# Performance work log

Measured on AMD Instinct MI355X. Metric: run time of the kernel, lower is better.

## Reference

```python
import jax, jax.numpy as jnp
import numpy as np
import math

B, S, HID = 2, 1024, 2048
NH, HD = 16, 128
STREAM_R, SELECT_R, RECENT_R = 0.02, 0.06, 0.08
FF = 0.9  # forgetting factor
ROPE_BASE = 10000.0


def setup_inputs() -> dict:
    key = jax.random.key(0)
    ks = jax.random.split(key, 5)
    return {
        "hidden_states": jax.random.normal(ks[0], (B, S, HID), dtype=jnp.float32),
        "wq": jax.random.normal(ks[1], (HID, HID), dtype=jnp.float32) * 0.02,
        "wk": jax.random.normal(ks[2], (HID, HID), dtype=jnp.float32) * 0.02,
        "wv": jax.random.normal(ks[3], (HID, HID), dtype=jnp.float32) * 0.02,
        "wo": jax.random.normal(ks[4], (HID, HID), dtype=jnp.float32) * 0.02,
    }


def _rope_tables(seq_len, dim):
    inv_freq = 1.0 / (ROPE_BASE ** (jnp.arange(0, dim, 2, dtype=jnp.float32) / dim))
    freqs = jnp.outer(jnp.arange(seq_len, dtype=jnp.float32), inv_freq)  # [S, D/2]
    emb = jnp.concatenate([freqs, freqs], axis=-1)  # [S, D]
    return jnp.cos(emb), jnp.sin(emb)


def _rotate_half(x):
    x1, x2 = jnp.split(x, 2, axis=-1)
    return jnp.concatenate([-x2, x1], axis=-1)


def a2s_base_mask(attn_weights, sb, selb, rb, ff):
    # attn_weights: [B,H,S,S] (causal mask already added). Returns bool keep-mask [B,H,S,S].
    Bv, Hv, Sq, Sk = attn_weights.shape
    scores = jax.nn.softmax(attn_weights.astype(jnp.float32), axis=-1)  # [B,H,S,S]
    cb = sb + selb + rb  # cache budget
    # EMA warmup over first cb rows: sum_i ff^(cb-1-i) * scores[i]
    w = ff ** jnp.arange(cb - 1, -1, -1, dtype=jnp.float32)
    select0 = jnp.einsum('t,bhts->bhs', w, scores[:, :, :cb, :])
    mask0 = jnp.ones((Bv, Hv, Sk), dtype=bool)
    pos = jnp.arange(Sk)

    xs_scores = jnp.moveaxis(scores[:, :, cb:Sk - 1, :], 2, 0)  # [T,B,H,S]
    ts = jnp.arange(cb, Sk - 1, dtype=jnp.int32)

    def step(carry, inp):
        sel, m = carry
        sc, t = inp
        cur = sc * m
        cur = cur / jnp.sum(cur, axis=-1, keepdims=True)
        sel = ff * sel + cur
        local = t - rb
        # argmin over window [sb : local+1]; outside -> +inf (evicted entries already +inf)
        win = jnp.where((pos >= sb) & (pos <= local), sel, jnp.inf)
        mi = jnp.argmin(win, axis=-1)  # [B,H], first-min like torch
        evict = pos == mi[..., None]  # [B,H,S] one-hot bool
        sel = jnp.where(evict, jnp.inf, sel)
        m_new = m & ~evict
        return (sel, m_new), m_new

    _, rows = jax.lax.scan(step, (select0, mask0), (xs_scores, ts))
    head = jnp.ones((Bv, Hv, cb + 1, Sk), dtype=bool)  # rows 0..cb stay all-True
    tail = jnp.moveaxis(rows, 0, 2)  # rows cb+1..S-1
    return jnp.concatenate([head, tail], axis=2)


def reference(hidden_states, wq, wk, wv, wo):
    sb = math.floor(STREAM_R * S + 0.5)
    selb = math.floor(SELECT_R * S + 0.5)
    rb = math.floor(RECENT_R * S + 0.5)

    q = (hidden_states @ wq).reshape(B, S, NH, HD).transpose(0, 2, 1, 3)
    k = (hidden_states @ wk).reshape(B, S, NH, HD).transpose(0, 2, 1, 3)
    v = (hidden_states @ wv).reshape(B, S, NH, HD).transpose(0, 2, 1, 3)

    cos, sin = _rope_tables(S, HD)  # [S,HD]
    q = q * cos + _rotate_half(q) * sin
    k = k * cos + _rotate_half(k) * sin

    attn = jnp.einsum('bhqd,bhkd->bhqk', q, k) / math.sqrt(HD)
    mask_val = jnp.finfo(jnp.float32).min
    causal = jnp.where(jnp.tril(jnp.ones((S, S), dtype=bool)), 0.0, mask_val)[None, None]
    attn = jnp.maximum(attn + causal, mask_val)

    keep = a2s_base_mask(jax.lax.stop_gradient(attn), sb, selb, rb, FF)
    attn = jnp.where(keep, attn, mask_val)  # torch.min(attention_mask) == mask_val

    probs = jax.nn.softmax(attn.astype(jnp.float32), axis=-1).astype(q.dtype)
    out = jnp.einsum('bhqk,bhkd->bhqd', probs, v)
    out = out.transpose(0, 2, 1, 3).reshape(B, S, HID)
    return out @ wo
```

## Files before the change

kernel.cpp:

```cpp
#include <hip/hip_runtime.h>
#include <math.h>

#define Bb    2
#define Ss    1024
#define HIDd  2048
#define NHh   16
#define HDd   128
#define SBc   20
#define SELBc 61
#define RBc   82
#define CBc   163
#define FFf   0.9f
#define MASKVAL (-3.4028234663852886e38f)
#define NBH   (Bb*NHh)
#define NROWS (NBH*Ss)

typedef __attribute__((ext_vector_type(8))) short short8;
typedef __attribute__((ext_vector_type(4))) float f32x4;

__device__ __forceinline__ unsigned short f2b(float f) {
    unsigned u = __float_as_uint(f);
    u = (u + 0x7FFFu + ((u >> 16) & 1u)) >> 16;
    return (unsigned short)u;
}
__device__ __forceinline__ float b2f(unsigned short h) {
    return __uint_as_float((unsigned)h << 16);
}

#if defined(__has_builtin)
#if __has_builtin(__builtin_amdgcn_global_load_lds)
#define USE_GLD 1
#endif
#endif

__device__ __forceinline__ void gload16(const void* g, void* l) {
#ifdef USE_GLD
    __builtin_amdgcn_global_load_lds(
        (const __attribute__((address_space(1))) void*)g,
        (__attribute__((address_space(3))) void*)l, 16, 0, 0);
#else
    *(short8*)l = *(const short8*)g;
#endif
}

__global__ __launch_bounds__(256) void conv_split(const float* __restrict__ x,
                                                  unsigned short* __restrict__ yh,
                                                  unsigned short* __restrict__ yl, int n4)
{
    int i = blockIdx.x * 256 + threadIdx.x;
    if (i >= n4) return;
    float4 v = ((const float4*)x)[i];
    ushort4 h, l;
    h.x = f2b(v.x); l.x = f2b(v.x - b2f(h.x));
    h.y = f2b(v.y); l.y = f2b(v.y - b2f(h.y));
    h.z = f2b(v.z); l.z = f2b(v.z - b2f(h.z));
    h.w = f2b(v.w); l.w = f2b(v.w - b2f(h.w));
    ((ushort4*)yh)[i] = h;
    ((ushort4*)yl)[i] = l;
}

__global__ __launch_bounds__(256) void tconv_all(const float* __restrict__ wq,
                                                 const float* __restrict__ wk,
                                                 const float* __restrict__ wv,
                                                 const float* __restrict__ wo,
                                                 unsigned short* __restrict__ wqth,
                                                 unsigned short* __restrict__ wqtl,
                                                 unsigned short* __restrict__ wkth,
                                                 unsigned short* __restrict__ wktl,
                                                 unsigned short* __restrict__ wvt,
                                                 unsigned short* __restrict__ wot)
{
    __shared__ float T[64][65];
    const int z = blockIdx.z;
    const float* W = (z == 0) ? wq : (z == 1) ? wk : (z == 2) ? wv : wo;
    int n0 = blockIdx.x * 64, k0 = blockIdx.y * 64;
    int tid = threadIdx.x;
    int rr = tid >> 4, cc = (tid & 15) * 4;
#pragma unroll
    for (int p = 0; p < 4; ++p) {
        int r = rr + p * 16;
        float4 x = *(const float4*)&W[(size_t)(k0 + r) * HIDd + n0 + cc];
        T[r][cc] = x.x; T[r][cc + 1] = x.y; T[r][cc + 2] = x.z; T[r][cc + 3] = x.w;
    }
    __syncthreads();
    if (z < 2) {
        unsigned short* Wth = z ? wkth : wqth;
        unsigned short* Wtl = z ? wktl : wqtl;
#pragma unroll
        for (int p = 0; p < 4; ++p) {
            int rn = rr + p * 16;
            float v0 = T[cc][rn], v1 = T[cc + 1][rn], v2 = T[cc + 2][rn], v3 = T[cc + 3][rn];
            ushort4 h, l;
            h.x = f2b(v0); l.x = f2b(v0 - b2f(h.x));
            h.y = f2b(v1); l.y = f2b(v1 - b2f(h.y));
            h.z = f2b(v2); l.z = f2b(v2 - b2f(h.z));
            h.w = f2b(v3); l.w = f2b(v3 - b2f(h.w));
            *(ushort4*)&Wth[(size_t)(n0 + rn) * HIDd + k0 + cc] = h;
            *(ushort4*)&Wtl[(size_t)(n0 + rn) * HIDd + k0 + cc] = l;
        }
    } else {
        unsigned short* Wt = (z == 2) ? wvt : wot;
#pragma unroll
        for (int p = 0; p < 4; ++p) {
            int rn = rr + p * 16;
            ushort4 o;
            o.x = f2b(T[cc][rn]);     o.y = f2b(T[cc + 1][rn]);
            o.z = f2b(T[cc + 2][rn]); o.w = f2b(T[cc + 3][rn]);
            *(ushort4*)&Wt[(size_t)(n0 + rn) * HIDd + k0 + cc] = o;
        }
    }
}

__global__ __launch_bounds__(256) void gemm_qkv(const unsigned short* __restrict__ hsh,
                                                const unsigned short* __restrict__ hsl,
                                                const unsigned short* __restrict__ wqth,
                                                const unsigned short* __restrict__ wqtl,
                                                const unsigned short* __restrict__ wkth,
                                                const unsigned short* __restrict__ wktl,
                                                const unsigned short* __restrict__ wvt,
                                                float* __restrict__ qf,
                                                float* __restrict__ kf,
                                                float* __restrict__ vf)
{
    __shared__ unsigned short AsH[128 * 32], AsL[128 * 32];
    __shared__ unsigned short BsH[128 * 32], BsL[128 * 32];
    const int tid = threadIdx.x;
    const int region = blockIdx.x >> 4;
    const int bn = (blockIdx.x & 15) * 128;
    const int bm = blockIdx.y * 128;
    const int K = HIDd;
    const int lane = tid & 63, wid = tid >> 6;
    const int wr = (wid >> 1) * 64, wc = (wid & 1) * 64;
    const int lm = lane & 15, lk = (lane >> 4) * 8;
    const int lr = (lane >> 4) * 4;

    f32x4 acc[4][4];
#pragma unroll
    for (int mi = 0; mi < 4; ++mi)
#pragma unroll
        for (int ni = 0; ni < 4; ++ni) acc[mi][ni] = 0.0f;

    if (region < 2) {
        const unsigned short* Bh = region ? wkth : wqth;
        const unsigned short* Bl = region ? wktl : wqtl;
        float* C = region ? kf : qf;
        for (int k0 = 0; k0 < K; k0 += 32) {
#pragma unroll
            for (int l = 0; l < 2; ++l) {
                int L = tid + l * 256;
                int row = L >> 2, c8 = (L & 3) * 8;
                size_t ga = (size_t)(bm + row) * K + k0 + c8;
                size_t gb = (size_t)(bn + row) * K + k0 + c8;
                gload16(&hsh[ga], &AsH[L * 8]);
                gload16(&hsl[ga], &AsL[L * 8]);
                gload16(&Bh[gb], &BsH[L * 8]);
                gload16(&Bl[gb], &BsL[L * 8]);
            }
            __syncthreads();
            short8 ah[4], al[4], bh[4], bl[4];
#pragma unroll
            for (int mi = 0; mi < 4; ++mi) {
                ah[mi] = *(short8*)&AsH[(wr + mi * 16 + lm) * 32 + lk];
                al[mi] = *(short8*)&AsL[(wr + mi * 16 + lm) * 32 + lk];
            }
#pragma unroll
            for (int ni = 0; ni < 4; ++ni) {
                bh[ni] = *(short8*)&BsH[(wc + ni * 16 + lm) * 32 + lk];
                bl[ni] = *(short8*)&BsL[(wc + ni * 16 + lm) * 32 + lk];
            }
#pragma unroll
            for (int mi = 0; mi < 4; ++mi)
#pragma unroll
                for (int ni = 0; ni < 4; ++ni) {
                    acc[mi][ni] = __builtin_amdgcn_mfma_f32_16x16x32_bf16(ah[mi], bh[ni], acc[mi][ni], 0, 0, 0);
                    acc[mi][ni] = __builtin_amdgcn_mfma_f32_16x16x32_bf16(ah[mi], bl[ni], acc[mi][ni], 0, 0, 0);
                    acc[mi][ni] = __builtin_amdgcn_mfma_f32_16x16x32_bf16(al[mi], bh[ni], acc[mi][ni], 0, 0, 0);
                }
            __syncthreads();
        }
#pragma unroll
        for (int mi = 0; mi < 4; ++mi)
#pragma unroll
            for (int ni = 0; ni < 4; ++ni)
#pragma unroll
                for (int r = 0; r < 4; ++r) {
                    int m = bm + wr + mi * 16 + lr + r;
                    int n = bn + wc + ni * 16 + lm;
                    int b_ = m / Ss, s_ = m % Ss;
                    int h_ = n / HDd, d_ = n % HDd;
                    C[(size_t)((b_ * NHh + h_) * Ss + s_) * HDd + d_] = acc[mi][ni][r];
                }
    } else {
        for (int k0 = 0; k0 < K; k0 += 32) {
#pragma unroll
            for (int l = 0; l < 2; ++l) {
                int L = tid + l * 256;
                int row = L >> 2, c8 = (L & 3) * 8;
                gload16(&hsh[(size_t)(bm + row) * K + k0 + c8], &AsH[L * 8]);
                gload16(&wvt[(size_t)(bn + row) * K + k0 + c8], &BsH[L * 8]);
            }
            __syncthreads();
            short8 af[4], bf[4];
#pragma unroll
            for (int mi = 0; mi < 4; ++mi) af[mi] = *(short8*)&AsH[(wr + mi * 16 + lm) * 32 + lk];
#pragma unroll
            for (int ni = 0; ni < 4; ++ni) bf[ni] = *(short8*)&BsH[(wc + ni * 16 + lm) * 32 + lk];
#pragma unroll
            for (int mi = 0; mi < 4; ++mi)
#pragma unroll
                for (int ni = 0; ni < 4; ++ni)
                    acc[mi][ni] = __builtin_amdgcn_mfma_f32_16x16x32_bf16(af[mi], bf[ni], acc[mi][ni], 0, 0, 0);
            __syncthreads();
        }
#pragma unroll
        for (int mi = 0; mi < 4; ++mi)
#pragma unroll
            for (int ni = 0; ni < 4; ++ni)
#pragma unroll
                for (int r = 0; r < 4; ++r) {
                    int m = bm + wr + mi * 16 + lr + r;
                    int n = bn + wc + ni * 16 + lm;
                    int b_ = m / Ss, s_ = m % Ss;
                    int h_ = n / HDd, d_ = n % HDd;
                    vf[(size_t)((b_ * NHh + h_) * Ss + s_) * HDd + d_] = acc[mi][ni][r];
                }
    }
}

__global__ __launch_bounds__(256) void gemm_bf16t(const unsigned short* __restrict__ A,
                                                  const unsigned short* __restrict__ Bt,
                                                  float* __restrict__ C,
                                                  int M, int N, int K)
{
    __shared__ unsigned short As[128 * 32];
    __shared__ unsigned short Bs[128 * 32];
    const int tid = threadIdx.x;
    const int bm = blockIdx.y * 128, bn = blockIdx.x * 128;
    const int lane = tid & 63, wid = tid >> 6;
    const int wr = (wid >> 1) * 64, wc = (wid & 1) * 64;
    const int lm = lane & 15, lk = (lane >> 4) * 8;

    f32x4 acc[4][4];
#pragma unroll
    for (int mi = 0; mi < 4; ++mi)
#pragma unroll
        for (int ni = 0; ni < 4; ++ni) acc[mi][ni] = 0.0f;

    for (int k0 = 0; k0 < K; k0 += 32) {
#pragma unroll
        for (int l = 0; l < 2; ++l) {
            int L = tid + l * 256;
            int row = L >> 2, c8 = (L & 3) * 8;
            gload16(&A[(size_t)(bm + row) * K + k0 + c8], &As[L * 8]);
            gload16(&Bt[(size_t)(bn + row) * K + k0 + c8], &Bs[L * 8]);
        }
        __syncthreads();
        short8 af[4], bf[4];
#pragma unroll
        for (int mi = 0; mi < 4; ++mi) af[mi] = *(short8*)&As[(wr + mi * 16 + lm) * 32 + lk];
#pragma unroll
        for (int ni = 0; ni < 4; ++ni) bf[ni] = *(short8*)&Bs[(wc + ni * 16 + lm) * 32 + lk];
#pragma unroll
        for (int mi = 0; mi < 4; ++mi)
#pragma unroll
            for (int ni = 0; ni < 4; ++ni)
                acc[mi][ni] = __builtin_amdgcn_mfma_f32_16x16x32_bf16(af[mi], bf[ni], acc[mi][ni], 0, 0, 0);
        __syncthreads();
    }
    const int lr = (lane >> 4) * 4;
#pragma unroll
    for (int mi = 0; mi < 4; ++mi)
#pragma unroll
        for (int ni = 0; ni < 4; ++ni)
#pragma unroll
            for (int r = 0; r < 4; ++r) {
                int m = bm + wr + mi * 16 + lr + r;
                int n = bn + wc + ni * 16 + lm;
                C[(size_t)m * N + n] = acc[mi][ni][r];
            }
}

__global__ __launch_bounds__(64) void rope_qk_split(const float* __restrict__ q,
                                                    const float* __restrict__ k,
                                                    unsigned short* __restrict__ qh,
                                                    unsigned short* __restrict__ ql,
                                                    unsigned short* __restrict__ kh,
                                                    unsigned short* __restrict__ kl)
{
    int idx = blockIdx.x;
    int s = idx % Ss;
    int d = threadIdx.x;
    float inv = powf(10000.0f, -2.0f * (float)d / 128.0f);
    float fr = (float)s * inv;
    float c = cosf(fr), sn = sinf(fr);
    size_t base = (size_t)idx * HDd;
    float q1 = q[base + d], q2 = q[base + d + 64];
    float k1 = k[base + d], k2 = k[base + d + 64];
    float qa = q1 * c - q2 * sn, qbv = q2 * c + q1 * sn;
    float ka = k1 * c - k2 * sn, kbv = k2 * c + k1 * sn;
    unsigned short h;
    h = f2b(qa);  qh[base + d]      = h; ql[base + d]      = f2b(qa  - b2f(h));
    h = f2b(qbv); qh[base + d + 64] = h; ql[base + d + 64] = f2b(qbv - b2f(h));
    h = f2b(ka);  kh[base + d]      = h; kl[base + d]      = f2b(ka  - b2f(h));
    h = f2b(kbv); kh[base + d + 64] = h; kl[base + d + 64] = f2b(kbv - b2f(h));
}

__global__ __launch_bounds__(256) void attn_qk_split(const unsigned short* __restrict__ qh,
                                                     const unsigned short* __restrict__ ql,
                                                     const unsigned short* __restrict__ kh,
                                                     const unsigned short* __restrict__ kl,
                                                     float* __restrict__ attn)
{
    const int bh = blockIdx.z;
    const int bm = blockIdx.y * 128, bn = blockIdx.x * 128;
    float* C = attn + (size_t)bh * Ss * Ss;
    const int tid = threadIdx.x;

    if (blockIdx.x > blockIdx.y) return;

    const size_t hb = (size_t)bh * Ss * HDd;
    const unsigned short* Ah = qh + hb;
    const unsigned short* Al = ql + hb;
    const unsigned short* Bh = kh + hb;
    const unsigned short* Bl = kl + hb;

    __shared__ unsigned short AsH[128 * 32], AsL[128 * 32];
    __shared__ unsigned short BsH[128 * 32], BsL[128 * 32];
    const int lane = tid & 63, wid = tid >> 6;
    const int wr = (wid >> 1) * 64, wc = (wid & 1) * 64;
    const int lm = lane & 15, lk = (lane >> 4) * 8;

    f32x4 acc[4][4];
#pragma unroll
    for (int mi = 0; mi < 4; ++mi)
#pragma unroll
        for (int ni = 0; ni < 4; ++ni) acc[mi][ni] = 0.0f;

    for (int k0 = 0; k0 < HDd; k0 += 32) {
#pragma unroll
        for (int l = 0; l < 2; ++l) {
            int L = tid + l * 256;
            int row = L >> 2, c8 = (L & 3) * 8;
            size_t ga = (size_t)(bm + row) * HDd + k0 + c8;
            size_t gb = (size_t)(bn + row) * HDd + k0 + c8;
            gload16(&Ah[ga], &AsH[L * 8]);
            gload16(&Al[ga], &AsL[L * 8]);
            gload16(&Bh[gb], &BsH[L * 8]);
            gload16(&Bl[gb], &BsL[L * 8]);
        }
        __syncthreads();
        short8 ah[4], al[4], bh2[4], bl2[4];
#pragma unroll
        for (int mi = 0; mi < 4; ++mi) {
            ah[mi] = *(short8*)&AsH[(wr + mi * 16 + lm) * 32 + lk];
            al[mi] = *(short8*)&AsL[(wr + mi * 16 + lm) * 32 + lk];
        }
#pragma unroll
        for (int ni = 0; ni < 4; ++ni) {
            bh2[ni] = *(short8*)&BsH[(wc + ni * 16 + lm) * 32 + lk];
            bl2[ni] = *(short8*)&BsL[(wc + ni * 16 + lm) * 32 + lk];
        }
#pragma unroll
        for (int mi = 0; mi < 4; ++mi)
#pragma unroll
            for (int ni = 0; ni < 4; ++ni) {
                acc[mi][ni] = __builtin_amdgcn_mfma_f32_16x16x32_bf16(ah[mi], bh2[ni], acc[mi][ni], 0, 0, 0);
                acc[mi][ni] = __builtin_amdgcn_mfma_f32_16x16x32_bf16(ah[mi], bl2[ni], acc[mi][ni], 0, 0, 0);
                acc[mi][ni] = __builtin_amdgcn_mfma_f32_16x16x32_bf16(al[mi], bh2[ni], acc[mi][ni], 0, 0, 0);
            }
        __syncthreads();
    }
    const float scale = 0.08838834764831845f;
    const int lr = (lane >> 4) * 4;
#pragma unroll
    for (int mi = 0; mi < 4; ++mi)
#pragma unroll
        for (int ni = 0; ni < 4; ++ni)
#pragma unroll
            for (int r = 0; r < 4; ++r) {
                int sq = bm + wr + mi * 16 + lr + r;
                int sk = bn + wc + ni * 16 + lm;
                C[(size_t)sq * Ss + sk] = (sk <= sq) ? acc[mi][ni][r] * scale : MASKVAL;
            }
}

__global__ __launch_bounds__(256) void softmax_rows(float* __restrict__ attn)
{
    int row = blockIdx.x;
    int r = row & (Ss - 1);
    float4* a4 = (float4*)(attn + (size_t)row * Ss);
    int tid = threadIdx.x;
    bool act = (tid * 4 <= r);
    float4 x = make_float4(MASKVAL, MASKVAL, MASKVAL, MASKVAL);
    if (act) x = a4[tid];
    float m = fmaxf(fmaxf(x.x, x.y), fmaxf(x.z, x.w));
#pragma unroll
    for (int off = 32; off; off >>= 1) m = fmaxf(m, __shfl_xor(m, off));
    __shared__ float red[4];
    if ((tid & 63) == 0) red[tid >> 6] = m;
    __syncthreads();
    float mm = fmaxf(fmaxf(red[0], red[1]), fmaxf(red[2], red[3]));
    float e0 = expf(x.x - mm), e1 = expf(x.y - mm);
    float e2 = expf(x.z - mm), e3 = expf(x.w - mm);
    float s = e0 + e1 + e2 + e3;
#pragma unroll
    for (int off = 32; off; off >>= 1) s += __shfl_xor(s, off);
    __shared__ float red2[4];
    if ((tid & 63) == 0) red2[tid >> 6] = s;
    __syncthreads();
    float inv = 1.0f / (red2[0] + red2[1] + red2[2] + red2[3]);
    a4[tid] = make_float4(e0 * inv, e1 * inv, e2 * inv, e3 * inv);
}

template<int CTRL>
__device__ __forceinline__ int dpp_i(int x) {
    return __builtin_amdgcn_update_dpp(0, x, CTRL, 0xF, 0xF, true);
}
__device__ __forceinline__ float wave_sum64(float x) {
    x += __int_as_float(dpp_i<0xB1>(__float_as_int(x)));
    x += __int_as_float(dpp_i<0x4E>(__float_as_int(x)));
    x += __int_as_float(dpp_i<0x141>(__float_as_int(x)));
    x += __int_as_float(dpp_i<0x140>(__float_as_int(x)));
    int xi = __float_as_int(x);
    float a = __int_as_float(__builtin_amdgcn_readlane(xi, 0));
    float b = __int_as_float(__builtin_amdgcn_readlane(xi, 16));
    float c = __int_as_float(__builtin_amdgcn_readlane(xi, 32));
    float d = __int_as_float(__builtin_amdgcn_readlane(xi, 48));
    return (a + c) + (b + d);
}

__device__ __forceinline__ unsigned long long u64min(unsigned long long a, unsigned long long b) {
    return a < b ? a : b;
}
template<int CTRL>
__device__ __forceinline__ unsigned long long dpp64(unsigned long long x) {
    int lo = (int)(unsigned)x;
    int hi = (int)(unsigned)(x >> 32);
    unsigned l2 = (unsigned)dpp_i<CTRL>(lo);
    unsigned h2 = (unsigned)dpp_i<CTRL>(hi);
    return ((unsigned long long)h2 << 32) | (unsigned long long)l2;
}
__device__ __forceinline__ unsigned long long wave_min64k(unsigned long long x) {
    x = u64min(x, dpp64<0xB1>(x));
    x = u64min(x, dpp64<0x4E>(x));
    x = u64min(x, dpp64<0x141>(x));
    x = u64min(x, dpp64<0x140>(x));
    int lo = (int)(unsigned)x;
    int hi = (int)(unsigned)(x >> 32);
    unsigned long long a = ((unsigned long long)(unsigned)__builtin_amdgcn_readlane(hi, 0)  << 32) |
                           (unsigned long long)(unsigned)__builtin_amdgcn_readlane(lo, 0);
    unsigned long long b = ((unsigned long long)(unsigned)__builtin_amdgcn_readlane(hi, 16) << 32) |
                           (unsigned long long)(unsigned)__builtin_amdgcn_readlane(lo, 16);
    unsigned long long c = ((unsigned long long)(unsigned)__builtin_amdgcn_readlane(hi, 32) << 32) |
                           (unsigned long long)(unsigned)__builtin_amdgcn_readlane(lo, 32);
    unsigned long long d = ((unsigned long long)(unsigned)__builtin_amdgcn_readlane(hi, 48) << 32) |
                           (unsigned long long)(unsigned)__builtin_amdgcn_readlane(lo, 48);
    return u64min(u64min(a, b), u64min(c, d));
}

__device__ __forceinline__ float f4c(float4 v, int i) {
    return i == 0 ? v.x : (i == 1 ? v.y : (i == 2 ? v.z : v.w));
}

template<int NC, int NCL>
__device__ __forceinline__ void scan_step(int t, int lane,
                                          const float4* __restrict__ A4,
                                          unsigned char* __restrict__ KP,
                                          float4 (&rb)[4],
                                          float (&sel)[4][4],
                                          float (&mf)[4][4])
{
    const float INFv = __int_as_float(0x7f800000);
    float4 a[NC];
#pragma unroll
    for (int jj = 0; jj < NC; ++jj) a[jj] = rb[jj];
    int tp = t + 4; if (tp > Ss - 1) tp = Ss - 1;
#pragma unroll
    for (int jj = 0; jj < NCL; ++jj) rb[jj] = A4[tp * 256 + jj * 64 + lane];

    float lsum = 0.0f;
#pragma unroll
    for (int jj = 0; jj < NC; ++jj) {
        float c0 = a[jj].x * mf[jj][0], c1 = a[jj].y * mf[jj][1];
        float c2 = a[jj].z * mf[jj][2], c3 = a[jj].w * mf[jj][3];
        lsum += (c0 + c1) + (c2 + c3);
    }
    float tot = wave_sum64(lsum);
    float inv = 1.0f / tot;

    const int local = t - RBc;
    const int base = lane * 4;
    const bool ge = (base >= SBc);

    unsigned long long kmin = 0xFFFFFFFFFFFFFFFFull;
#pragma unroll
    for (int jj = 0; jj < NC; ++jj) {
        unsigned long long kk[4];
#pragma unroll
        for (int i = 0; i < 4; ++i) {
            float sv = fmaf(FFf, sel[jj][i], f4c(a[jj], i) * inv);
            sel[jj][i] = sv;
            int s = jj * 256 + base + i;
            bool win = (s <= local) && (jj > 0 || ge);
            unsigned hi = win ? __float_as_uint(sv) : 0x7f800000u;
            kk[i] = ((unsigned long long)hi << 32) | (unsigned long long)(unsigned)s;
        }
        unsigned long long cm = u64min(u64min(kk[0], kk[1]), u64min(kk[2], kk[3]));
        kmin = u64min(kmin, cm);
    }
    kmin = wave_min64k(kmin);
    const int besti = (int)(unsigned)(kmin & 0xFFFFFFFFull);

#pragma unroll
    for (int jj = 0; jj < NC; ++jj)
#pragma unroll
        for (int i = 0; i < 4; ++i) {
            int s = jj * 256 + base + i;
            bool e = (s == besti);
            sel[jj][i] = e ? INFv : sel[jj][i];
            mf[jj][i]  = e ? 0.0f : mf[jj][i];
        }

    uchar4* kp4 = (uchar4*)(KP + (size_t)(t + 1) * Ss);
#pragma unroll
    for (int jj = 0; jj < NC; ++jj) {
        uchar4 kb;
        kb.x = (unsigned char)mf[jj][0];
        kb.y = (unsigned char)mf[jj][1];
        kb.z = (unsigned char)mf[jj][2];
        kb.w = (unsigned char)mf[jj][3];
        kp4[jj * 64 + lane] = kb;
    }
}

__global__ __launch_bounds__(64) void scan_kernel5(const float* __restrict__ scores,
                                                   unsigned char* __restrict__ keep)
{
    int bh = blockIdx.x;
    int lane = threadIdx.x;
    const float4* A4 = (const float4*)(scores + (size_t)bh * Ss * Ss);
    unsigned char* KP = keep + (size_t)bh * Ss * Ss;

    float sel[4][4];
    float mf[4][4];
#pragma unroll
    for (int jj = 0; jj < 4; ++jj)
#pragma unroll
        for (int i = 0; i < 4; ++i) { sel[jj][i] = 0.0f; mf[jj][i] = 1.0f; }

    float4 w0 = A4[0 * 256 + lane];
    float4 w1 = A4[1 * 256 + lane];
    float4 w2 = A4[2 * 256 + lane];
    float4 w3 = A4[3 * 256 + lane];
#define WSTEP(W, NEXT)                                                       \
    do {                                                                     \
        float4 _a = W;                                                       \
        W = A4[(NEXT) * 256 + lane];                                         \
        sel[0][0] = fmaf(FFf, sel[0][0], _a.x);                              \
        sel[0][1] = fmaf(FFf, sel[0][1], _a.y);                              \
        sel[0][2] = fmaf(FFf, sel[0][2], _a.z);                              \
        sel[0][3] = fmaf(FFf, sel[0][3], _a.w);                              \
    } while (0)
    for (int r = 0; r < 160; r += 4) {
        WSTEP(w0, r + 4); WSTEP(w1, r + 5); WSTEP(w2, r + 6); WSTEP(w3, r + 7);
    }
#undef WSTEP
    {
        float4 tl[3] = { w0, w1, w2 };
#pragma unroll
        for (int u = 0; u < 3; ++u) {
            sel[0][0] = fmaf(FFf, sel[0][0], tl[u].x);
            sel[0][1] = fmaf(FFf, sel[0][1], tl[u].y);
            sel[0][2] = fmaf(FFf, sel[0][2], tl[u].z);
            sel[0][3] = fmaf(FFf, sel[0][3], tl[u].w);
        }
    }

    float4 rb[4][4];
#pragma unroll
    for (int slot = 0; slot < 4; ++slot)
        rb[slot][0] = A4[(163 + slot) * 256 + lane];

    for (int t0 = 163; t0 < 255; t0 += 4) {
        scan_step<1, 2>(t0 + 0, lane, A4, KP, rb[0], sel, mf);
        scan_step<1, 2>(t0 + 1, lane, A4, KP, rb[1], sel, mf);
        scan_step<1, 2>(t0 + 2, lane, A4, KP, rb[2], sel, mf);
        scan_step<1, 2>(t0 + 3, lane, A4, KP, rb[3], sel, mf);
    }
    for (int t0 = 255; t0 < 511; t0 += 4) {
        scan_step<2, 3>(t0 + 0, lane, A4, KP, rb[0], sel, mf);
        scan_step<2, 3>(t0 + 1, lane, A4, KP, rb[1], sel, mf);
        scan_step<2, 3>(t0 + 2, lane, A4, KP, rb[2], sel, mf);
        scan_step<2, 3>(t0 + 3, lane, A4, KP, rb[3], sel, mf);
    }
    for (int t0 = 511; t0 < 767; t0 += 4) {
        scan_step<3, 4>(t0 + 0, lane, A4, KP, rb[0], sel, mf);
        scan_step<3, 4>(t0 + 1, lane, A4, KP, rb[1], sel, mf);
        scan_step<3, 4>(t0 + 2, lane, A4, KP, rb[2], sel, mf);
        scan_step<3, 4>(t0 + 3, lane, A4, KP, rb[3], sel, mf);
    }
    for (int t0 = 767; t0 < 1023; t0 += 4) {
        scan_step<4, 4>(t0 + 0, lane, A4, KP, rb[0], sel, mf);
        scan_step<4, 4>(t0 + 1, lane, A4, KP, rb[1], sel, mf);
        scan_step<4, 4>(t0 + 2, lane, A4, KP, rb[2], sel, mf);
        scan_step<4, 4>(t0 + 3, lane, A4, KP, rb[3], sel, mf);
    }
}

__global__ __launch_bounds__(256) void pv_renorm(const float* __restrict__ scores,
                                                 const unsigned char* __restrict__ keep,
                                                 const float* __restrict__ v,
                                                 unsigned short* __restrict__ ctxb)
{
    int bh = blockIdx.z;
    int b_ = bh / NHh, h_ = bh % NHh;
    const float* P = scores + (size_t)bh * Ss * Ss;
    const unsigned char* KPm = keep + (size_t)bh * Ss * Ss;
    const float* V = v + (size_t)bh * Ss * HDd;
    int bm = blockIdx.y * 64, bn = blockIdx.x * 64;
    int tid = threadIdx.x, tx = tid & 15, ty = tid >> 4;
    __shared__ float As[16][65];
    __shared__ float Bs[16][64];
    float acc[4][4] = {};
    float rs[4] = {};
    int kend = bm + 64;
    for (int k0 = 0; k0 < kend; k0 += 16) {
#pragma unroll
        for (int l = 0; l < 4; ++l) {
            int idx = tid + l * 256;
            int r = idx >> 4, c = idx & 15;
            int row = bm + r;
            float p = P[(size_t)row * Ss + k0 + c];
            if (row > CBc && !KPm[(size_t)row * Ss + k0 + c]) p = 0.0f;
            As[c][r] = p;
        }
#pragma unroll
        for (int l = 0; l < 4; ++l) {
            int idx = tid + l * 256;
            int r = idx >> 6, c = idx & 63;
            Bs[r][c] = V[(size_t)(k0 + r) * HDd + bn + c];
        }
        __syncthreads();
#pragma unroll
        for (int kk = 0; kk < 16; ++kk) {
            float a[4], b[4];
#pragma unroll
            for (int i = 0; i < 4; ++i) a[i] = As[kk][ty * 4 + i];
#pragma unroll
            for (int j = 0; j < 4; ++j) b[j] = Bs[kk][tx * 4 + j];
#pragma unroll
            for (int i = 0; i < 4; ++i) rs[i] += a[i];
#pragma unroll
            for (int i = 0; i < 4; ++i)
#pragma unroll
                for (int j = 0; j < 4; ++j)
                    acc[i][j] = fmaf(a[i], b[j], acc[i][j]);
        }
        __syncthreads();
    }
#pragma unroll
    for (int i = 0; i < 4; ++i) {
        float inv = 1.0f / rs[i];
        int sq = bm + ty * 4 + i;
#pragma unroll
        for (int j = 0; j < 4; ++j) {
            int d = bn + tx * 4 + j;
            ctxb[(size_t)(b_ * Ss + sq) * HIDd + h_ * HDd + d] = f2b(acc[i][j] * inv);
        }
    }
}

extern "C" void kernel_launch(void* const* d_in, const int* in_sizes, int n_in,
                              void* d_out, int out_size, void* d_ws, size_t ws_size,
                              hipStream_t stream)
{
    const float* hs = (const float*)d_in[0];
    const float* wq = (const float*)d_in[1];
    const float* wk = (const float*)d_in[2];
    const float* wv = (const float*)d_in[3];
    const float* wo = (const float*)d_in[4];
    float* out = (float*)d_out;

    float* ws = (float*)d_ws;
    size_t off = 0;
    float* qf   = ws + off; off += (size_t)NBH * Ss * HDd;
    float* kf   = ws + off; off += (size_t)NBH * Ss * HDd;
    float* vf   = ws + off; off += (size_t)NBH * Ss * HDd;
    float* attn = ws + off; off += (size_t)NBH * Ss * Ss;
    unsigned char* keep = (unsigned char*)(ws + off); off += (size_t)NBH * Ss * Ss / 4;
    unsigned short* wot = (unsigned short*)(ws + off); off += (size_t)HIDd * HIDd / 2;

    unsigned short* hsh  = (unsigned short*)(attn);
    unsigned short* hsl  = (unsigned short*)(attn + 2u * 1024 * 1024);
    unsigned short* wqth = (unsigned short*)(attn + 4u * 1024 * 1024);
    unsigned short* wqtl = (unsigned short*)(attn + 6u * 1024 * 1024);
    unsigned short* wkth = (unsigned short*)(attn + 8u * 1024 * 1024);
    unsigned short* wktl = (unsigned short*)(attn + 10u * 1024 * 1024);
    unsigned short* wvt  = (unsigned short*)(attn + 12u * 1024 * 1024);
    unsigned short* qh = (unsigned short*)keep;
    unsigned short* ql = (unsigned short*)(keep + 8u * 1024 * 1024);
    unsigned short* kh = (unsigned short*)(keep + 16u * 1024 * 1024);
    unsigned short* kl = (unsigned short*)(keep + 24u * 1024 * 1024);
    unsigned short* ctxb = (unsigned short*)qf;

    dim3 blk(256);
    const int M = Bb * Ss;

    conv_split<<<dim3((M * HIDd / 4 + 255) / 256), blk, 0, stream>>>(hs, hsh, hsl, M * HIDd / 4);

    tconv_all<<<dim3(HIDd / 64, HIDd / 64, 4), blk, 0, stream>>>(
        wq, wk, wv, wo, wqth, wqtl, wkth, wktl, wvt, wot);

    gemm_qkv<<<dim3(48, M / 128), blk, 0, stream>>>(
        hsh, hsl, wqth, wqtl, wkth, wktl, wvt, qf, kf, vf);

    rope_qk_split<<<dim3(NBH * Ss), dim3(64), 0, stream>>>(qf, kf, qh, ql, kh, kl);

    attn_qk_split<<<dim3(Ss / 128, Ss / 128, NBH), blk, 0, stream>>>(qh, ql, kh, kl, attn);

    softmax_rows<<<dim3(NROWS), blk, 0, stream>>>(attn);

    scan_kernel5<<<dim3(NBH), dim3(64), 0, stream>>>(attn, keep);

    pv_renorm<<<dim3(HDd / 64, Ss / 64, NBH), blk, 0, stream>>>(attn, keep, vf, ctxb);

    gemm_bf16t<<<dim3(HIDd / 128, M / 128), blk, 0, stream>>>(ctxb, wot, out, M, HIDd, HIDd);
}
```

Before: 985.9 us.

## Load QK MFMA fragments directly from global and vectorize PV shared reads

The split-bf16 QK^T kernel no longer stages Q/K tiles through shared memory with barriers. Each wave now loads its MFMA fragments straight from global memory into registers and relies on the cache for reuse, with the k-loop fully unrolled. Separately, the PV kernel pads its shared A tile to 68 columns so rows stay 16-byte aligned, and reads A and B as float4 vectors. The global-load path risks redundant traffic, since fragments are reused across waves only through the cache, and higher register pressure from the unrolled loop.

```diff
diff --git a/kernel.cpp b/kernel.cpp
--- a/kernel.cpp
+++ b/kernel.cpp
@@ -313,19 +313,12 @@
 {
     const int bh = blockIdx.z;
     const int bm = blockIdx.y * 128, bn = blockIdx.x * 128;
+    const int tid = threadIdx.x;
+
+    if (blockIdx.x > blockIdx.y) return;
+
     float* C = attn + (size_t)bh * Ss * Ss;
-    const int tid = threadIdx.x;
-
-    if (blockIdx.x > blockIdx.y) return;
-
     const size_t hb = (size_t)bh * Ss * HDd;
-    const unsigned short* Ah = qh + hb;
-    const unsigned short* Al = ql + hb;
-    const unsigned short* Bh = kh + hb;
-    const unsigned short* Bl = kl + hb;
-
-    __shared__ unsigned short AsH[128 * 32], AsL[128 * 32];
-    __shared__ unsigned short BsH[128 * 32], BsL[128 * 32];
     const int lane = tid & 63, wid = tid >> 6;
     const int wr = (wid >> 1) * 64, wc = (wid & 1) * 64;
     const int lm = lane & 15, lk = (lane >> 4) * 8;
@@ -336,29 +329,20 @@
 #pragma unroll
         for (int ni = 0; ni < 4; ++ni) acc[mi][ni] = 0.0f;
 
+#pragma unroll
     for (int k0 = 0; k0 < HDd; k0 += 32) {
-#pragma unroll
-        for (int l = 0; l < 2; ++l) {
-            int L = tid + l * 256;
-            int row = L >> 2, c8 = (L & 3) * 8;
-            size_t ga = (size_t)(bm + row) * HDd + k0 + c8;
-            size_t gb = (size_t)(bn + row) * HDd + k0 + c8;
-            gload16(&Ah[ga], &AsH[L * 8]);
-            gload16(&Al[ga], &AsL[L * 8]);
-            gload16(&Bh[gb], &BsH[L * 8]);
-            gload16(&Bl[gb], &BsL[L * 8]);
-        }
-        __syncthreads();
         short8 ah[4], al[4], bh2[4], bl2[4];
 #pragma unroll
         for (int mi = 0; mi < 4; ++mi) {
-            ah[mi] = *(short8*)&AsH[(wr + mi * 16 + lm) * 32 + lk];
-            al[mi] = *(short8*)&AsL[(wr + mi * 16 + lm) * 32 + lk];
+            size_t ra = hb + (size_t)(bm + wr + mi * 16 + lm) * HDd + k0 + lk;
+            ah[mi] = *(const short8*)&qh[ra];
+            al[mi] = *(const short8*)&ql[ra];
         }
 #pragma unroll
         for (int ni = 0; ni < 4; ++ni) {
-            bh2[ni] = *(short8*)&BsH[(wc + ni * 16 + lm) * 32 + lk];
-            bl2[ni] = *(short8*)&BsL[(wc + ni * 16 + lm) * 32 + lk];
+            size_t rb = hb + (size_t)(bn + wc + ni * 16 + lm) * HDd + k0 + lk;
+            bh2[ni] = *(const short8*)&kh[rb];
+            bl2[ni] = *(const short8*)&kl[rb];
         }
 #pragma unroll
         for (int mi = 0; mi < 4; ++mi)
@@ -368,7 +352,6 @@
                 acc[mi][ni] = __builtin_amdgcn_mfma_f32_16x16x32_bf16(ah[mi], bl2[ni], acc[mi][ni], 0, 0, 0);
                 acc[mi][ni] = __builtin_amdgcn_mfma_f32_16x16x32_bf16(al[mi], bh2[ni], acc[mi][ni], 0, 0, 0);
             }
-        __syncthreads();
     }
     const float scale = 0.08838834764831845f;
     const int lr = (lane >> 4) * 4;
@@ -619,7 +602,7 @@
     const float* V = v + (size_t)bh * Ss * HDd;
     int bm = blockIdx.y * 64, bn = blockIdx.x * 64;
     int tid = threadIdx.x, tx = tid & 15, ty = tid >> 4;
-    __shared__ float As[16][65];
+    __shared__ float As[16][68];
     __shared__ float Bs[16][64];
     float acc[4][4] = {};
     float rs[4] = {};
@@ -643,11 +626,10 @@
         __syncthreads();
 #pragma unroll
         for (int kk = 0; kk < 16; ++kk) {
-            float a[4], b[4];
-#pragma unroll
-            for (int i = 0; i < 4; ++i) a[i] = As[kk][ty * 4 + i];
-#pragma unroll
-            for (int j = 0; j < 4; ++j) b[j] = Bs[kk][tx * 4 + j];
+            float4 av = *(const float4*)&As[kk][ty * 4];
+            float4 bv = *(const float4*)&Bs[kk][tx * 4];
+            float a[4] = { av.x, av.y, av.z, av.w };
+            float b[4] = { bv.x, bv.y, bv.z, bv.w };
 #pragma unroll
             for (int i = 0; i < 4; ++i) rs[i] += a[i];
 #pragma unroll
```

Result: slower. 1.008 ms (+2.3%).
